# Kernel optimization log

Hardware: AMD Instinct MI355X
Metric: run time of the kernel (lower is better)

The kernel has to match this reference:

```python
import jax, jax.numpy as jnp
import numpy as np
from jax import lax

B, R, F = 100, 15, 4096       # batch, regions, feature dim
V, E, D, A, T = 10000, 1024, 1024, 512, 500  # vocab, embed, decoder, attention, topic
LIN = 1024                    # autoencoder linear output width
NT = 5                        # sentences per paragraph
L = 52                        # max caption length


def setup_inputs() -> dict:
    key = jax.random.key(0)
    ks = jax.random.split(key, 16)
    g = lambda i, shp, s: jax.random.normal(ks[i], shp, jnp.float32) * s
    return {
        "image_features": g(0, (B, R, F), 1.0),
        "encoded_captions": jax.random.randint(ks[1], (B, NT, L), 0, V),
        "caption_lengths": jax.random.randint(ks[2], (B, NT), 1, L),
        # autoencoder
        "W_lt": g(3, (LIN, F), 0.02), "b_lt": jnp.zeros((LIN,), jnp.float32),
        "conv_w": g(4, (6, 1, 15, 26), 0.05), "conv_b": jnp.zeros((6,), jnp.float32),
        # attention MLP (weight_norm linears == plain linears mathematically)
        "W_feat": g(5, (A, F), 0.02), "b_feat": jnp.zeros((A,), jnp.float32),
        "W_dec": g(6, (A, D), 0.02), "b_dec": jnp.zeros((A,), jnp.float32),
        "W_top": g(7, (A, T), 0.02), "b_top": jnp.zeros((A,), jnp.float32),
        "W_full": g(8, (1, A), 0.02), "b_full": jnp.zeros((1,), jnp.float32),
        # embedding + LSTM cells + output heads
        "emb": g(9, (V, E), 0.1),
        "W_ih1": g(10, (4 * D, E + F + D), 0.01), "W_hh1": g(11, (4 * D, D), 0.01),
        "b_ih1": jnp.zeros((4 * D,), jnp.float32), "b_hh1": jnp.zeros((4 * D,), jnp.float32),
        "W_ih2": g(12, (4 * D, F + D), 0.01), "W_hh2": g(13, (4 * D, D), 0.01),
        "b_ih2": jnp.zeros((4 * D,), jnp.float32), "b_hh2": jnp.zeros((4 * D,), jnp.float32),
        "W_fc1": g(14, (V, D), 0.02), "b_fc1": jnp.zeros((V,), jnp.float32),
        "W_fc": g(15, (V, D), 0.02), "b_fc": jnp.zeros((V,), jnp.float32),
    }


def _lstm_cell(x, h, c, W_ih, W_hh, b_ih, b_hh):
    gates = x @ W_ih.T + b_ih + h @ W_hh.T + b_hh
    i, f, g_, o = jnp.split(gates, 4, axis=-1)
    c = jax.nn.sigmoid(f) * c + jax.nn.sigmoid(i) * jnp.tanh(g_)
    h = jax.nn.sigmoid(o) * jnp.tanh(c)
    return h, c


def reference(image_features, encoded_captions, caption_lengths, W_lt, b_lt,
              conv_w, conv_b, W_feat, b_feat, W_dec, b_dec, W_top, b_top,
              W_full, b_full, emb, W_ih1, W_hh1, b_ih1, b_hh1,
              W_ih2, W_hh2, b_ih2, b_hh2, W_fc1, b_fc1, W_fc, b_fc):
    def per_sample(img, caps, lens):
        # img (R,F), caps (NT,L) int, lens (NT,) int
        img_mean = img.mean(0)  # (F,)
        # autoencoder: linear 4096->1024, conv2d(1->6, k=(15,26), stride 2)
        x = (img @ W_lt.T + b_lt)[None, None]  # (1,1,R,LIN)
        conv = lax.conv_general_dilated(x, conv_w, (2, 2), "VALID",
                                        dimension_numbers=("NCHW", "OIHW", "NCHW"))
        topics = conv[0, :, 0, :] + conv_b[:, None]  # (6, T=500)
        att1 = img @ W_feat.T + b_feat               # (R,A), precomputed once
        # last word of each sentence: caps[t, lens[t]-1]
        last_words = jnp.take_along_axis(caps, (lens - 1)[:, None], axis=1)[:, 0]  # (NT,)
        last_embs = emb[last_words]                  # (NT,E)

        def step(carry, tup):
            h1, c1, h2, c2 = carry
            topic_t, emb_t = tup
            # top-down attention LSTM: cat([h2, img_mean, word_emb])
            x1 = jnp.concatenate([h2, img_mean, emb_t])
            h1, c1 = _lstm_cell(x1, h1, c1, W_ih1, W_hh1, b_ih1, b_hh1)
            # attention over R regions (dropout is identity in eval)
            att = jax.nn.relu(att1 + (h1 @ W_dec.T + b_dec) + (topic_t @ W_top.T + b_top))
            scores = att @ W_full[0] + b_full[0]     # (R,)
            alpha = jax.nn.softmax(scores)
            awe = alpha @ img                        # (F,)
            preds1 = h1 @ W_fc1.T + b_fc1            # (V,)
            h2, c2 = _lstm_cell(jnp.concatenate([awe, h1]), h2, c2,
                                W_ih2, W_hh2, b_ih2, b_hh2)
            preds = h2 @ W_fc.T + b_fc               # (V,)
            return (h1, c1, h2, c2), (preds, preds1)

        z = jnp.zeros((D,), img.dtype)
        _, (preds, preds1) = lax.scan(step, (z, z, z, z), (topics[:NT], last_embs))
        return preds, preds1                          # (NT,V) each

    preds, preds1 = jax.vmap(per_sample)(image_features, encoded_captions, caption_lengths)
    return preds, preds1, encoded_captions, caption_lengths - 1
```

## Files before the change

kernel.cpp:

```cpp
#include <hip/hip_runtime.h>

typedef __attribute__((ext_vector_type(8))) short short8;
typedef __attribute__((ext_vector_type(4))) short short4v;
typedef __attribute__((ext_vector_type(4))) float f32x4;

__device__ __forceinline__ unsigned short f2bf(float f) {
  unsigned int u = __float_as_uint(f);
  u += 0x7fffu + ((u >> 16) & 1u);
  return (unsigned short)(u >> 16);
}
__device__ __forceinline__ float bf2f(unsigned short u) {
  return __uint_as_float(((unsigned int)u) << 16);
}
__device__ __forceinline__ float sigm(float x) { return 1.f / (1.f + expf(-x)); }

template<int NKC>
__global__ __launch_bounds__(256) void gemm_v5(
    const unsigned short* __restrict__ X, int ldx,
    const unsigned short* __restrict__ W, int ldw, int N,
    unsigned short* __restrict__ C, long long slotStride)
{
  __shared__ short8 lds[3584];
  const int tid = threadIdx.x;
  const int lane = tid & 63, wv = tid >> 6;
  const int l16 = lane & 15, kg = (lane >> 4) * 8;
  const int mbase = blockIdx.y * 112;
  const int ncol = blockIdx.x * 64 + wv * 16 + l16;
  const int nrow = (ncol < N) ? ncol : (N - 1);
  const long long k0 = (long long)blockIdx.z * (NKC * 256);
  C += (long long)blockIdx.z * slotStride;

  const unsigned short* wp = W + (size_t)nrow * ldw + kg + k0;
  const unsigned short* xb = X + (size_t)(mbase + l16) * ldx + kg + k0;
  const size_t xrow = (size_t)16 * ldx;

  f32x4 acc[7];
#pragma unroll
  for (int i = 0; i < 7; ++i) acc[i] = (f32x4){0.f, 0.f, 0.f, 0.f};

  for (int kc = 0; kc < NKC; ++kc) {
    if (kc) __syncthreads();
    short8 wbuf[8];
#pragma unroll
    for (int ks = 0; ks < 8; ++ks)
      wbuf[ks] = *(const short8*)(wp + kc * 256 + ks * 32);
    short8 xst[14];
#pragma unroll
    for (int i = 0; i < 14; ++i) {
      const int f = wv + i * 4, mt = f >> 3, ks = f & 7;
      xst[i] = *(const short8*)(xb + (size_t)mt * xrow + kc * 256 + ks * 32);
    }
#pragma unroll
    for (int i = 0; i < 14; ++i) lds[(wv + i * 4) * 64 + lane] = xst[i];
    __syncthreads();
#pragma unroll
    for (int ks = 0; ks < 8; ++ks)
#pragma unroll
      for (int mt = 0; mt < 7; ++mt) {
        short8 a = lds[(mt * 8 + ks) * 64 + lane];
        acc[mt] = __builtin_amdgcn_mfma_f32_16x16x32_bf16(a, wbuf[ks], acc[mt], 0, 0, 0);
      }
  }
  if (ncol < N) {
    const int r0 = (lane >> 4) * 4;
#pragma unroll
    for (int mt = 0; mt < 7; ++mt)
#pragma unroll
      for (int r = 0; r < 4; ++r)
        C[(size_t)(mbase + mt * 16 + r0 + r) * N + ncol] = f2bf(acc[mt][r]);
  }
}

template<int NKC>
__global__ __launch_bounds__(256) void gemm_v5f(
    const unsigned short* __restrict__ X, int ldx,
    const float* __restrict__ W, int ldw, int N,
    unsigned short* __restrict__ C, long long slotStride)
{
  __shared__ short8 lds[3584];
  const int tid = threadIdx.x;
  const int lane = tid & 63, wv = tid >> 6;
  const int l16 = lane & 15, kg = (lane >> 4) * 8;
  const int mbase = blockIdx.y * 112;
  const int ncol = blockIdx.x * 64 + wv * 16 + l16;
  const int nrow = (ncol < N) ? ncol : (N - 1);
  const long long k0 = (long long)blockIdx.z * (NKC * 256);
  C += (long long)blockIdx.z * slotStride;

  const float* wp = W + (size_t)nrow * ldw + kg + k0;
  const unsigned short* xb = X + (size_t)(mbase + l16) * ldx + kg + k0;
  const size_t xrow = (size_t)16 * ldx;

  f32x4 acc[7];
#pragma unroll
  for (int i = 0; i < 7; ++i) acc[i] = (f32x4){0.f, 0.f, 0.f, 0.f};

  for (int kc = 0; kc < NKC; ++kc) {
    if (kc) __syncthreads();
    float4 wa[8], wb[8];
#pragma unroll
    for (int ks = 0; ks < 8; ++ks) {
      wa[ks] = *(const float4*)(wp + kc * 256 + ks * 32);
      wb[ks] = *(const float4*)(wp + kc * 256 + ks * 32 + 4);
    }
    short8 xst[14];
#pragma unroll
    for (int i = 0; i < 14; ++i) {
      const int f = wv + i * 4, mt = f >> 3, ks = f & 7;
      xst[i] = *(const short8*)(xb + (size_t)mt * xrow + kc * 256 + ks * 32);
    }
#pragma unroll
    for (int i = 0; i < 14; ++i) lds[(wv + i * 4) * 64 + lane] = xst[i];
    __syncthreads();
#pragma unroll
    for (int ks = 0; ks < 8; ++ks) {
      short8 w;
      w[0] = (short)f2bf(wa[ks].x); w[1] = (short)f2bf(wa[ks].y);
      w[2] = (short)f2bf(wa[ks].z); w[3] = (short)f2bf(wa[ks].w);
      w[4] = (short)f2bf(wb[ks].x); w[5] = (short)f2bf(wb[ks].y);
      w[6] = (short)f2bf(wb[ks].z); w[7] = (short)f2bf(wb[ks].w);
#pragma unroll
      for (int mt = 0; mt < 7; ++mt) {
        short8 a = lds[(mt * 8 + ks) * 64 + lane];
        acc[mt] = __builtin_amdgcn_mfma_f32_16x16x32_bf16(a, w, acc[mt], 0, 0, 0);
      }
    }
  }
  if (ncol < N) {
    const int r0 = (lane >> 4) * 4;
#pragma unroll
    for (int mt = 0; mt < 7; ++mt)
#pragma unroll
      for (int r = 0; r < 4; ++r)
        C[(size_t)(mbase + mt * 16 + r0 + r) * N + ncol] = f2bf(acc[mt][r]);
  }
}

__global__ __launch_bounds__(256) void k_pack_all(
    const float* __restrict__ Wih1, const float* __restrict__ Whh1,
    const float* __restrict__ Wih2, const float* __restrict__ Whh2,
    const float* __restrict__ Wfc1, const float* __restrict__ Wdec,
    const float* __restrict__ Wfc,  const float* __restrict__ Wtop,
    unsigned short* __restrict__ Wg1, unsigned short* __restrict__ Wg2,
    unsigned short* __restrict__ Wcat, unsigned short* __restrict__ Wfcb,
    unsigned short* __restrict__ Wtopb)
{
  int i = blockIdx.x * 256 + threadIdx.x;
  float4 v; unsigned short* dst; long long di;
  if (i < 2097152) {
    int row = i >> 9, c4 = i & 511;
    const float* s = (c4 < 256) ? Wih1 + (size_t)row * 6144 + c4 * 4
                                : Whh1 + (size_t)row * 1024 + (c4 - 256) * 4;
    v = *(const float4*)s; dst = Wg1; di = i;
  } else if (i < 8388608) {
    int j = i - 2097152; int row = j / 1536, c4 = j - row * 1536;
    const float* s = (c4 < 1280) ? Wih2 + (size_t)row * 5120 + c4 * 4
                                 : Whh2 + (size_t)row * 1024 + (c4 - 1280) * 4;
    v = *(const float4*)s; dst = Wg2; di = j;
  } else if (i < 11079680) {
    int j = i - 8388608; int row = j >> 8, c4 = j & 255;
    const float* s = (row < 10000) ? Wfc1 + (size_t)row * 1024 + c4 * 4
                                   : Wdec + (size_t)(row - 10000) * 1024 + c4 * 4;
    v = *(const float4*)s; dst = Wcat; di = j;
  } else if (i < 13639680) { int j = i - 11079680; v = ((const float4*)Wfc)[j]; dst = Wfcb; di = j; }
  else {
    int j = i - 13639680; if (j >= 65536) return;
    int n = j >> 7, c4 = j & 127;
    v = (c4 < 125) ? *(const float4*)(Wtop + (size_t)n * 500 + c4 * 4)
                   : (float4){0.f, 0.f, 0.f, 0.f};
    dst = Wtopb; di = j;
  }
  short4v o; o[0] = (short)f2bf(v.x); o[1] = (short)f2bf(v.y);
  o[2] = (short)f2bf(v.z); o[3] = (short)f2bf(v.w);
  ((short4v*)dst)[di] = o;
}

__global__ __launch_bounds__(256) void k_ximg2(const float* __restrict__ img,
    unsigned short* __restrict__ Ximg, unsigned short* __restrict__ Xmean) {
  int idx = blockIdx.x * 256 + threadIdx.x;
  int b = idx >> 12, f = idx & 4095;
  float s = 0.f;
#pragma unroll
  for (int r = 0; r < 15; ++r) {
    float v = img[((size_t)(b * 15 + r) << 12) + f];
    s += v;
    Ximg[((size_t)(b * 15 + r) << 12) + f] = f2bf(v);
  }
  Xmean[((size_t)b << 12) + f] = f2bf(s * (1.f / 15.f));
}

__global__ __launch_bounds__(256) void k_reduce(const unsigned short* __restrict__ P,
    long long ss, int nslots, const float* __restrict__ bias, int colmask,
    float* __restrict__ out, int total) {
  int idx = blockIdx.x * 256 + threadIdx.x;
  if (idx >= total) return;
  float s = bias ? bias[idx & colmask] : 0.f;
  for (int sl = 0; sl < nslots; ++sl) s += bf2f(P[(size_t)sl * ss + idx]);
  out[idx] = s;
}

__global__ __launch_bounds__(512) void k_conv(const unsigned short* __restrict__ px,
    const float* __restrict__ blt, const float* __restrict__ cw,
    const float* __restrict__ cb, unsigned short* __restrict__ Xtop) {
  int b = blockIdx.x;
  __shared__ float L[15 * 1024];
  for (int i = threadIdx.x; i < 15 * 1024; i += 512) {
    float s = blt[i & 1023];
#pragma unroll
    for (int sl = 0; sl < 8; ++sl)
      s += bf2f(px[(size_t)sl * 1605632 + (size_t)b * 15360 + i]);
    L[i] = s;
  }
  __syncthreads();
  for (int idx = threadIdx.x; idx < 2500; idx += 512) {
    int tt = idx / 500, w = idx - tt * 500;
    float s = cb[tt];
    for (int kh = 0; kh < 15; ++kh) {
      const float* lr = &L[kh * 1024 + 2 * w];
      const float* wr = &cw[(tt * 15 + kh) * 26];
#pragma unroll
      for (int kw = 0; kw < 26; ++kw) s += lr[kw] * wr[kw];
    }
    Xtop[((size_t)(b * 5 + tt)) * 512 + w] = f2bf(s);
  }
}

__global__ __launch_bounds__(256) void k_gw(const int* __restrict__ caps,
    const int* __restrict__ lens, const float* __restrict__ emb,
    unsigned short* __restrict__ Xemb, float* __restrict__ out2,
    float* __restrict__ out3) {
  int idx = blockIdx.x * 256 + threadIdx.x;
  int bt = idx >> 10, e = idx & 1023;
  if (bt < 500) {
    int w = caps[bt * 52 + lens[bt] - 1];
    Xemb[idx] = f2bf(emb[(size_t)w * 1024 + e]);
  } else if (bt < 560) Xemb[idx] = 0;
  if (idx < 26000) out2[idx] = (float)caps[idx];
  if (idx < 500) out3[idx] = (float)(lens[idx] - 1);
}

__global__ __launch_bounds__(256) void k_gbase1(const unsigned short* __restrict__ P,
    const float* __restrict__ bih, const float* __restrict__ bhh,
    float* __restrict__ gb) {
  int idx = blockIdx.x * 256 + threadIdx.x;
  int m = idx >> 12, n = idx & 4095;
  float s = bih[n] + bhh[n];
#pragma unroll
  for (int sl = 0; sl < 8; ++sl) s += bf2f(P[((size_t)sl * 112 + m) * 4096 + n]);
  gb[idx] = s;
}

__global__ __launch_bounds__(256) void k_lstm1(const unsigned short* __restrict__ P,
    const float* __restrict__ gb1, const float* __restrict__ gemb, int t,
    float* __restrict__ c1, unsigned short* __restrict__ Xh1,
    unsigned short* __restrict__ X1, unsigned short* __restrict__ X2) {
  int idx = blockIdx.x * 256 + threadIdx.x;
  int b = idx >> 10, j = idx & 1023;
  float g[4];
#pragma unroll
  for (int x = 0; x < 4; ++x) {
    int col = (x << 10) + j;
    float s = gb1[b * 4096 + col] + gemb[((size_t)b * 5 + t) * 4096 + col];
#pragma unroll
    for (int sl = 0; sl < 8; ++sl) s += bf2f(P[((size_t)sl * 112 + b) * 4096 + col]);
    g[x] = s;
  }
  float c = sigm(g[1]) * c1[idx] + sigm(g[0]) * tanhf(g[2]);
  float h = sigm(g[3]) * tanhf(c);
  c1[idx] = c;
  unsigned short hb = f2bf(h);
  Xh1[idx] = hb;
  X1[b * 2048 + 1024 + j] = hb;
  X2[(size_t)b * 6144 + 4096 + j] = hb;
}

__global__ __launch_bounds__(256) void k_attpred(const float* __restrict__ att1,
    const unsigned short* __restrict__ px, const float* __restrict__ bdec,
    const float* __restrict__ btop, const unsigned short* __restrict__ ttopb,
    const float* __restrict__ wfull, int t,
    const unsigned short* __restrict__ Ximg, unsigned short* __restrict__ X2,
    const float* __restrict__ bfc1, float* __restrict__ outp) {
  if (blockIdx.x >= 100) {
    int idx = (blockIdx.x - 100) * 256 + threadIdx.x;
    if (idx >= 1000000) return;
    int b = idx / 10000, v = idx - b * 10000;
    outp[((size_t)b * 5 + t) * 10000 + v] = bfc1[v]
        + bf2f(px[(size_t)b * 10512 + v])         + bf2f(px[(size_t)(112 + b) * 10512 + v])
        + bf2f(px[(size_t)(224 + b) * 10512 + v]) + bf2f(px[(size_t)(336 + b) * 10512 + v]);
    return;
  }
  int b = blockIdx.x;
  int tid = threadIdx.x;
  int r = tid & 15, ch = tid >> 4;
  __shared__ float sp[16][17];
  __shared__ float al[16];
  float s = 0.f;
  if (r < 15) {
    const float* a1 = att1 + ((size_t)b * 15 + r) * 512;
    const unsigned short* tp = ttopb + ((size_t)b * 5 + t) * 512;
#pragma unroll
    for (int j = 0; j < 32; ++j) {
      int n = ch * 32 + j;
      float ad = bdec[n] + btop[n]
               + bf2f(px[((size_t)0 * 112 + b) * 10512 + 10000 + n])
               + bf2f(px[((size_t)1 * 112 + b) * 10512 + 10000 + n])
               + bf2f(px[((size_t)2 * 112 + b) * 10512 + 10000 + n])
               + bf2f(px[((size_t)3 * 112 + b) * 10512 + 10000 + n]);
      float v = a1[n] + ad + bf2f(tp[n]);
      s += fmaxf(v, 0.f) * wfull[n];
    }
  }
  sp[r][ch] = s;
  __syncthreads();
  if (tid == 0) {
    float sc[15];
    float m = -1e30f;
    for (int rr = 0; rr < 15; ++rr) {
      float x = 0.f;
      for (int cc = 0; cc < 16; ++cc) x += sp[rr][cc];
      sc[rr] = x; m = fmaxf(m, x);
    }
    float sum = 0.f;
    for (int rr = 0; rr < 15; ++rr) { sc[rr] = expf(sc[rr] - m); sum += sc[rr]; }
    float inv = 1.f / sum;
    for (int rr = 0; rr < 15; ++rr) al[rr] = sc[rr] * inv;
  }
  __syncthreads();
  for (int f = tid; f < 4096; f += 256) {
    float s2 = 0.f;
#pragma unroll
    for (int rr = 0; rr < 15; ++rr)
      s2 += al[rr] * bf2f(Ximg[((size_t)b * 15 + rr) * 4096 + f]);
    X2[(size_t)b * 6144 + f] = f2bf(s2);
  }
}

__global__ __launch_bounds__(256) void k_lstm2(const unsigned short* __restrict__ P,
    const float* __restrict__ bih, const float* __restrict__ bhh,
    float* __restrict__ c2, unsigned short* __restrict__ Xh2,
    unsigned short* __restrict__ X1, unsigned short* __restrict__ X2) {
  int idx = blockIdx.x * 256 + threadIdx.x;
  int b = idx >> 10, j = idx & 1023;
  float g[4];
#pragma unroll
  for (int x = 0; x < 4; ++x) {
    int col = (x << 10) + j;
    float s = bih[col] + bhh[col];
#pragma unroll
    for (int sl = 0; sl < 12; ++sl) s += bf2f(P[((size_t)sl * 112 + b) * 4096 + col]);
    g[x] = s;
  }
  float c = sigm(g[1]) * c2[idx] + sigm(g[0]) * tanhf(g[2]);
  float h = sigm(g[3]) * tanhf(c);
  c2[idx] = c;
  unsigned short hb = f2bf(h);
  Xh2[idx] = hb;
  X1[b * 2048 + j] = hb;
  X2[(size_t)b * 6144 + 5120 + j] = hb;
}

__global__ __launch_bounds__(256) void k_eppred(const unsigned short* __restrict__ P,
    const float* __restrict__ bias, float* __restrict__ outp, int t, int ldp) {
  int idx = blockIdx.x * 256 + threadIdx.x;
  if (idx >= 1000000) return;
  int b = idx / 10000, v = idx - b * 10000;
  outp[((size_t)b * 5 + t) * 10000 + v] = bias[v]
      + bf2f(P[(size_t)b * ldp + v])         + bf2f(P[(size_t)(112 + b) * ldp + v])
      + bf2f(P[(size_t)(224 + b) * ldp + v]) + bf2f(P[(size_t)(336 + b) * ldp + v]);
}

extern "C" void kernel_launch(void* const* d_in, const int* in_sizes, int n_in,
                              void* d_out, int out_size, void* d_ws, size_t ws_size,
                              hipStream_t stream) {
  (void)in_sizes; (void)n_in; (void)out_size;
  const float* imgf  = (const float*)d_in[0];
  const int*   caps  = (const int*)d_in[1];
  const int*   lens  = (const int*)d_in[2];
  const float* W_lt  = (const float*)d_in[3];
  const float* b_lt  = (const float*)d_in[4];
  const float* convw = (const float*)d_in[5];
  const float* convb = (const float*)d_in[6];
  const float* W_feat = (const float*)d_in[7];
  const float* b_feat = (const float*)d_in[8];
  const float* W_dec = (const float*)d_in[9];
  const float* b_dec = (const float*)d_in[10];
  const float* W_top = (const float*)d_in[11];
  const float* b_top = (const float*)d_in[12];
  const float* W_full = (const float*)d_in[13];
  const float* b_full = (const float*)d_in[14];  (void)b_full;
  const float* emb   = (const float*)d_in[15];
  const float* W_ih1 = (const float*)d_in[16];
  const float* W_hh1 = (const float*)d_in[17];
  const float* b_ih1 = (const float*)d_in[18];
  const float* b_hh1 = (const float*)d_in[19];
  const float* W_ih2 = (const float*)d_in[20];
  const float* W_hh2 = (const float*)d_in[21];
  const float* b_ih2 = (const float*)d_in[22];
  const float* b_hh2 = (const float*)d_in[23];
  const float* W_fc1 = (const float*)d_in[24];
  const float* b_fc1 = (const float*)d_in[25];
  const float* W_fc  = (const float*)d_in[26];
  const float* b_fc  = (const float*)d_in[27];
  float* out = (float*)d_out;

  char* ws = (char*)d_ws;
  size_t off = 0;
  auto alloc = [&](size_t bytes) -> size_t {
    size_t o = off; off = (off + bytes + 255) & ~(size_t)255; return o;
  };
  const size_t oZERO  = off;
  const size_t oXimg  = alloc(1568ull * 4096 * 2);
  const size_t oXmean = alloc(112ull * 4096 * 2);
  const size_t oX1    = alloc(112ull * 2048 * 2);
  const size_t oX2    = alloc(112ull * 6144 * 2);
  const size_t oXh1   = alloc(112ull * 1024 * 2);
  const size_t oXh2   = alloc(112ull * 1024 * 2);
  const size_t oc1    = alloc(100ull * 1024 * 4);
  const size_t oc2    = alloc(100ull * 1024 * 4);
  const size_t oXtop  = alloc(560ull * 512 * 2);
  const size_t zeroBytes = off - oZERO;
  const size_t oXemb  = alloc(560ull * 1024 * 2);
  const size_t oTtopb = alloc(560ull * 512 * 2);
  const size_t oatt1  = alloc(1568ull * 512 * 4);
  const size_t ogb1   = alloc(112ull * 4096 * 4);
  const size_t ogemb  = alloc(560ull * 4096 * 4);
  const size_t opg    = alloc(12ull * 112 * 4096 * 2);
  const size_t opx    = alloc(8ull * 1568 * 1024 * 2);
  const size_t oWg1   = alloc(4096ull * 2048 * 2);
  const size_t oWg2   = alloc(4096ull * 6144 * 2);
  const size_t oWcat  = alloc(10512ull * 1024 * 2);
  const size_t oWfcb  = alloc(10000ull * 1024 * 2);
  const size_t oWtopb = alloc(512ull * 512 * 2);
  if (ws_size < off) return;

  unsigned short* Ximg  = (unsigned short*)(ws + oXimg);
  unsigned short* Xmean = (unsigned short*)(ws + oXmean);
  unsigned short* Xemb  = (unsigned short*)(ws + oXemb);
  unsigned short* X1    = (unsigned short*)(ws + oX1);
  unsigned short* X2    = (unsigned short*)(ws + oX2);
  unsigned short* Xh1   = (unsigned short*)(ws + oXh1);
  unsigned short* Xh2   = (unsigned short*)(ws + oXh2);
  float* c1    = (float*)(ws + oc1);
  float* c2    = (float*)(ws + oc2);
  unsigned short* Xtop  = (unsigned short*)(ws + oXtop);
  unsigned short* Ttopb = (unsigned short*)(ws + oTtopb);
  float* att1  = (float*)(ws + oatt1);
  float* gb1   = (float*)(ws + ogb1);
  float* gemb  = (float*)(ws + ogemb);
  unsigned short* pg    = (unsigned short*)(ws + opg);
  unsigned short* px    = (unsigned short*)(ws + opx);
  unsigned short* Wg1   = (unsigned short*)(ws + oWg1);
  unsigned short* Wg2   = (unsigned short*)(ws + oWg2);
  unsigned short* Wcat  = (unsigned short*)(ws + oWcat);
  unsigned short* Wfcb  = (unsigned short*)(ws + oWfcb);
  unsigned short* Wtopb = (unsigned short*)(ws + oWtopb);

  const long long S4  = 112ll * 4096;
  const long long SP1 = 112ll * 10512;
  const long long SP  = 112ll * 10000;

  hipMemsetAsync(ws + oZERO, 0, zeroBytes, stream);

  k_ximg2<<<1600, 256, 0, stream>>>(imgf, Ximg, Xmean);
  k_pack_all<<<53536, 256, 0, stream>>>(W_ih1, W_hh1, W_ih2, W_hh2, W_fc1, W_dec,
                                        W_fc, W_top, Wg1, Wg2, Wcat, Wfcb, Wtopb);
  gemm_v5f<2><<<dim3(16, 14, 8), 256, 0, stream>>>(Ximg, 4096, W_lt, 4096, 1024,
                                                   px, 1568ll * 1024);
  k_conv<<<100, 512, 0, stream>>>(px, b_lt, convw, convb, Xtop);
  gemm_v5<2><<<dim3(8, 5, 1), 256, 0, stream>>>(Xtop, 512, Wtopb, 512, 512, Ttopb, 0);
  gemm_v5f<2><<<dim3(8, 14, 8), 256, 0, stream>>>(Ximg, 4096, W_feat, 4096, 512,
                                                  px, 1568ll * 512);
  k_reduce<<<3136, 256, 0, stream>>>(px, 1568ll * 512, 8, b_feat, 511, att1, 1568 * 512);
  k_gw<<<2240, 256, 0, stream>>>(caps, lens, emb, Xemb, out + 10000000, out + 10026000);
  gemm_v5f<2><<<dim3(64, 1, 8), 256, 0, stream>>>(Xmean, 4096, W_ih1 + 1024, 6144, 4096,
                                                  pg, S4);
  k_gbase1<<<1792, 256, 0, stream>>>(pg, b_ih1, b_hh1, gb1);
  gemm_v5f<1><<<dim3(64, 5, 4), 256, 0, stream>>>(Xemb, 1024, W_ih1 + 5120, 6144, 4096,
                                                  px, 560ll * 4096);
  k_reduce<<<8960, 256, 0, stream>>>(px, 560ll * 4096, 4, nullptr, 4095, gemb, 560 * 4096);

  for (int t = 0; t < 5; ++t) {
    gemm_v5<1><<<dim3(64, 1, 8), 256, 0, stream>>>(X1, 2048, Wg1, 2048, 4096, pg, S4);
    k_lstm1<<<400, 256, 0, stream>>>(pg, gb1, gemb, t, c1, Xh1, X1, X2);
    gemm_v5<1><<<dim3(165, 1, 4), 256, 0, stream>>>(Xh1, 1024, Wcat, 1024, 10512, px, SP1);
    k_attpred<<<4007, 256, 0, stream>>>(att1, px, b_dec, b_top, Ttopb, W_full, t,
                                        Ximg, X2, b_fc1, out + 5000000);
    gemm_v5<2><<<dim3(64, 1, 12), 256, 0, stream>>>(X2, 6144, Wg2, 6144, 4096, pg, S4);
    k_lstm2<<<400, 256, 0, stream>>>(pg, b_ih2, b_hh2, c2, Xh2, X1, X2);
    gemm_v5<1><<<dim3(157, 1, 4), 256, 0, stream>>>(Xh2, 1024, Wfcb, 1024, 10000, px, SP);
    k_eppred<<<3907, 256, 0, stream>>>(px, b_fc, out, t, 10000);
  }
}
```

Measured before the change: 688.6 us.

## Fuse preds epilogue into next step's gate GEMM and vectorize prep kernels

Adds a combined kernel that runs the layer-1 gate GEMM for step t and, in extra blocks, the reduction plus bias of the previous step's vocab logits. This removes one launch per step and lets the two independent pieces of work overlap. The final step's epilogue runs after the loop, and the fc partials get their own buffer so the next GEMM cannot overwrite them. The weight-pack and image-convert kernels now handle four elements per thread with float4/short4 accesses, which cuts the launched block count. Risk: the fused GEMM blocks and the elementwise reduction blocks have uneven costs inside one grid.

```diff
diff --git a/kernel.cpp b/kernel.cpp
--- a/kernel.cpp
+++ b/kernel.cpp
@@ -136,6 +136,66 @@
   }
 }
 
+__global__ __launch_bounds__(256) void k_g1ep(
+    const unsigned short* __restrict__ X1,
+    const unsigned short* __restrict__ Wg1,
+    unsigned short* __restrict__ pg, long long S4,
+    const unsigned short* __restrict__ pxp, const float* __restrict__ bfc,
+    float* __restrict__ outp, int tprev)
+{
+  __shared__ short8 lds[3584];
+  if (blockIdx.x >= 512) {
+    int idx = (blockIdx.x - 512) * 256 + threadIdx.x;
+    if (idx >= 1000000) return;
+    int b = idx / 10000, v = idx - b * 10000;
+    outp[((size_t)b * 5 + tprev) * 10000 + v] = bfc[v]
+        + bf2f(pxp[(size_t)b * 10000 + v])         + bf2f(pxp[(size_t)(112 + b) * 10000 + v])
+        + bf2f(pxp[(size_t)(224 + b) * 10000 + v]) + bf2f(pxp[(size_t)(336 + b) * 10000 + v]);
+    return;
+  }
+  const int bx = blockIdx.x & 63, bz = blockIdx.x >> 6;
+  const int tid = threadIdx.x;
+  const int lane = tid & 63, wv = tid >> 6;
+  const int l16 = lane & 15, kg = (lane >> 4) * 8;
+  const int ncol = bx * 64 + wv * 16 + l16;
+  const long long k0 = (long long)bz * 256;
+  unsigned short* C = pg + (long long)bz * S4;
+
+  const unsigned short* wp = Wg1 + (size_t)ncol * 2048 + kg + k0;
+  const unsigned short* xb = X1 + (size_t)l16 * 2048 + kg + k0;
+  const size_t xrow = (size_t)16 * 2048;
+
+  f32x4 acc[7];
+#pragma unroll
+  for (int i = 0; i < 7; ++i) acc[i] = (f32x4){0.f, 0.f, 0.f, 0.f};
+
+  short8 wbuf[8];
+#pragma unroll
+  for (int ks = 0; ks < 8; ++ks) wbuf[ks] = *(const short8*)(wp + ks * 32);
+  short8 xst[14];
+#pragma unroll
+  for (int i = 0; i < 14; ++i) {
+    const int f = wv + i * 4, mt = f >> 3, ks = f & 7;
+    xst[i] = *(const short8*)(xb + (size_t)mt * xrow + ks * 32);
+  }
+#pragma unroll
+  for (int i = 0; i < 14; ++i) lds[(wv + i * 4) * 64 + lane] = xst[i];
+  __syncthreads();
+#pragma unroll
+  for (int ks = 0; ks < 8; ++ks)
+#pragma unroll
+    for (int mt = 0; mt < 7; ++mt) {
+      short8 a = lds[(mt * 8 + ks) * 64 + lane];
+      acc[mt] = __builtin_amdgcn_mfma_f32_16x16x32_bf16(a, wbuf[ks], acc[mt], 0, 0, 0);
+    }
+  const int r0 = (lane >> 4) * 4;
+#pragma unroll
+  for (int mt = 0; mt < 7; ++mt)
+#pragma unroll
+    for (int r = 0; r < 4; ++r)
+      C[(size_t)(mt * 16 + r0 + r) * 4096 + ncol] = f2bf(acc[mt][r]);
+}
+
 __global__ __launch_bounds__(256) void k_pack_all(
     const float* __restrict__ Wih1, const float* __restrict__ Whh1,
     const float* __restrict__ Wih2, const float* __restrict__ Whh2,
@@ -145,48 +205,56 @@
     unsigned short* __restrict__ Wcat, unsigned short* __restrict__ Wfcb,
     unsigned short* __restrict__ Wtopb)
 {
-  int i = blockIdx.x * 256 + threadIdx.x;
-  float4 v; unsigned short* dst; long long di;
-  if (i < 2097152) {
-    int row = i >> 9, c4 = i & 511;
-    const float* s = (c4 < 256) ? Wih1 + (size_t)row * 6144 + c4 * 4
-                                : Whh1 + (size_t)row * 1024 + (c4 - 256) * 4;
-    v = *(const float4*)s; dst = Wg1; di = i;
-  } else if (i < 8388608) {
-    int j = i - 2097152; int row = j / 1536, c4 = j - row * 1536;
-    const float* s = (c4 < 1280) ? Wih2 + (size_t)row * 5120 + c4 * 4
-                                 : Whh2 + (size_t)row * 1024 + (c4 - 1280) * 4;
-    v = *(const float4*)s; dst = Wg2; di = j;
-  } else if (i < 11079680) {
-    int j = i - 8388608; int row = j >> 8, c4 = j & 255;
-    const float* s = (row < 10000) ? Wfc1 + (size_t)row * 1024 + c4 * 4
-                                   : Wdec + (size_t)(row - 10000) * 1024 + c4 * 4;
-    v = *(const float4*)s; dst = Wcat; di = j;
-  } else if (i < 13639680) { int j = i - 11079680; v = ((const float4*)Wfc)[j]; dst = Wfcb; di = j; }
-  else {
-    int j = i - 13639680; if (j >= 65536) return;
-    int n = j >> 7, c4 = j & 127;
-    v = (c4 < 125) ? *(const float4*)(Wtop + (size_t)n * 500 + c4 * 4)
-                   : (float4){0.f, 0.f, 0.f, 0.f};
-    dst = Wtopb; di = j;
-  }
-  short4v o; o[0] = (short)f2bf(v.x); o[1] = (short)f2bf(v.y);
-  o[2] = (short)f2bf(v.z); o[3] = (short)f2bf(v.w);
-  ((short4v*)dst)[di] = o;
+  const int base = (blockIdx.x * 256 + threadIdx.x) * 4;
+#pragma unroll
+  for (int u = 0; u < 4; ++u) {
+    const int i = base + u;
+    float4 v; unsigned short* dst; long long di;
+    if (i < 2097152) {
+      int row = i >> 9, c4 = i & 511;
+      const float* s = (c4 < 256) ? Wih1 + (size_t)row * 6144 + c4 * 4
+                                  : Whh1 + (size_t)row * 1024 + (c4 - 256) * 4;
+      v = *(const float4*)s; dst = Wg1; di = i;
+    } else if (i < 8388608) {
+      int j = i - 2097152; int row = j / 1536, c4 = j - row * 1536;
+      const float* s = (c4 < 1280) ? Wih2 + (size_t)row * 5120 + c4 * 4
+                                   : Whh2 + (size_t)row * 1024 + (c4 - 1280) * 4;
+      v = *(const float4*)s; dst = Wg2; di = j;
+    } else if (i < 11079680) {
+      int j = i - 8388608; int row = j >> 8, c4 = j & 255;
+      const float* s = (row < 10000) ? Wfc1 + (size_t)row * 1024 + c4 * 4
+                                     : Wdec + (size_t)(row - 10000) * 1024 + c4 * 4;
+      v = *(const float4*)s; dst = Wcat; di = j;
+    } else if (i < 13639680) { int j = i - 11079680; v = ((const float4*)Wfc)[j]; dst = Wfcb; di = j; }
+    else {
+      int j = i - 13639680; if (j >= 65536) continue;
+      int n = j >> 7, c4 = j & 127;
+      v = (c4 < 125) ? *(const float4*)(Wtop + (size_t)n * 500 + c4 * 4)
+                     : (float4){0.f, 0.f, 0.f, 0.f};
+      dst = Wtopb; di = j;
+    }
+    short4v o; o[0] = (short)f2bf(v.x); o[1] = (short)f2bf(v.y);
+    o[2] = (short)f2bf(v.z); o[3] = (short)f2bf(v.w);
+    ((short4v*)dst)[di] = o;
+  }
 }
 
 __global__ __launch_bounds__(256) void k_ximg2(const float* __restrict__ img,
     unsigned short* __restrict__ Ximg, unsigned short* __restrict__ Xmean) {
   int idx = blockIdx.x * 256 + threadIdx.x;
-  int b = idx >> 12, f = idx & 4095;
-  float s = 0.f;
+  int b = idx >> 10, f4 = idx & 1023;
+  float4 s = {0.f, 0.f, 0.f, 0.f};
 #pragma unroll
   for (int r = 0; r < 15; ++r) {
-    float v = img[((size_t)(b * 15 + r) << 12) + f];
-    s += v;
-    Ximg[((size_t)(b * 15 + r) << 12) + f] = f2bf(v);
-  }
-  Xmean[((size_t)b << 12) + f] = f2bf(s * (1.f / 15.f));
+    float4 v = *(const float4*)(img + (((size_t)(b * 15 + r)) << 12) + f4 * 4);
+    s.x += v.x; s.y += v.y; s.z += v.z; s.w += v.w;
+    short4v o; o[0] = (short)f2bf(v.x); o[1] = (short)f2bf(v.y);
+    o[2] = (short)f2bf(v.z); o[3] = (short)f2bf(v.w);
+    *(short4v*)(Ximg + (((size_t)(b * 15 + r)) << 12) + f4 * 4) = o;
+  }
+  short4v m; m[0] = (short)f2bf(s.x * (1.f / 15.f)); m[1] = (short)f2bf(s.y * (1.f / 15.f));
+  m[2] = (short)f2bf(s.z * (1.f / 15.f)); m[3] = (short)f2bf(s.w * (1.f / 15.f));
+  *(short4v*)(Xmean + (((size_t)b) << 12) + f4 * 4) = m;
 }
 
 __global__ __launch_bounds__(256) void k_reduce(const unsigned short* __restrict__ P,
@@ -426,6 +494,7 @@
   const size_t ogemb  = alloc(560ull * 4096 * 4);
   const size_t opg    = alloc(12ull * 112 * 4096 * 2);
   const size_t opx    = alloc(8ull * 1568 * 1024 * 2);
+  const size_t opp    = alloc(4ull * 112 * 10000 * 2);
   const size_t oWg1   = alloc(4096ull * 2048 * 2);
   const size_t oWg2   = alloc(4096ull * 6144 * 2);
   const size_t oWcat  = alloc(10512ull * 1024 * 2);
@@ -449,6 +518,7 @@
   float* gemb  = (float*)(ws + ogemb);
   unsigned short* pg    = (unsigned short*)(ws + opg);
   unsigned short* px    = (unsigned short*)(ws + opx);
+  unsigned short* pp    = (unsigned short*)(ws + opp);
   unsigned short* Wg1   = (unsigned short*)(ws + oWg1);
   unsigned short* Wg2   = (unsigned short*)(ws + oWg2);
   unsigned short* Wcat  = (unsigned short*)(ws + oWcat);
@@ -461,8 +531,8 @@
 
   hipMemsetAsync(ws + oZERO, 0, zeroBytes, stream);
 
-  k_ximg2<<<1600, 256, 0, stream>>>(imgf, Ximg, Xmean);
-  k_pack_all<<<53536, 256, 0, stream>>>(W_ih1, W_hh1, W_ih2, W_hh2, W_fc1, W_dec,
+  k_ximg2<<<400, 256, 0, stream>>>(imgf, Ximg, Xmean);
+  k_pack_all<<<13384, 256, 0, stream>>>(W_ih1, W_hh1, W_ih2, W_hh2, W_fc1, W_dec,
                                         W_fc, W_top, Wg1, Wg2, Wcat, Wfcb, Wtopb);
   gemm_v5f<2><<<dim3(16, 14, 8), 256, 0, stream>>>(Ximg, 4096, W_lt, 4096, 1024,
                                                    px, 1568ll * 1024);
@@ -480,14 +550,17 @@
   k_reduce<<<8960, 256, 0, stream>>>(px, 560ll * 4096, 4, nullptr, 4095, gemb, 560 * 4096);
 
   for (int t = 0; t < 5; ++t) {
-    gemm_v5<1><<<dim3(64, 1, 8), 256, 0, stream>>>(X1, 2048, Wg1, 2048, 4096, pg, S4);
+    if (t == 0)
+      gemm_v5<1><<<dim3(64, 1, 8), 256, 0, stream>>>(X1, 2048, Wg1, 2048, 4096, pg, S4);
+    else
+      k_g1ep<<<4419, 256, 0, stream>>>(X1, Wg1, pg, S4, pp, b_fc, out, t - 1);
     k_lstm1<<<400, 256, 0, stream>>>(pg, gb1, gemb, t, c1, Xh1, X1, X2);
     gemm_v5<1><<<dim3(165, 1, 4), 256, 0, stream>>>(Xh1, 1024, Wcat, 1024, 10512, px, SP1);
     k_attpred<<<4007, 256, 0, stream>>>(att1, px, b_dec, b_top, Ttopb, W_full, t,
                                         Ximg, X2, b_fc1, out + 5000000);
     gemm_v5<2><<<dim3(64, 1, 12), 256, 0, stream>>>(X2, 6144, Wg2, 6144, 4096, pg, S4);
     k_lstm2<<<400, 256, 0, stream>>>(pg, b_ih2, b_hh2, c2, Xh2, X1, X2);
-    gemm_v5<1><<<dim3(157, 1, 4), 256, 0, stream>>>(Xh2, 1024, Wfcb, 1024, 10000, px, SP);
-    k_eppred<<<3907, 256, 0, stream>>>(px, b_fc, out, t, 10000);
-  }
-}
+    gemm_v5<1><<<dim3(157, 1, 4), 256, 0, stream>>>(Xh2, 1024, Wfcb, 1024, 10000, pp, SP);
+  }
+  k_eppred<<<3907, 256, 0, stream>>>(pp, b_fc, out, 4, 10000);
+}
```

Result: slower. 834.9 us (+21.2%).
